# Kernel tuning notes

Hardware: AMD Instinct MI355X
Metric: run time of the kernel (lower is better)

## Reference

```python
import jax, jax.numpy as jnp
import numpy as np


def setup_inputs() -> dict:
    key = jax.random.key(0)
    ks = jax.random.split(key, 8)
    B, H, W, C = 4, 64, 64, 256
    d = C // 8  # 32
    s = 0.02
    return {
        "x": jax.random.normal(ks[0], (B, H, W, C), dtype=jnp.float32),
        "Wq": jax.random.normal(ks[1], (C, d), dtype=jnp.float32) * s,
        "bq": jnp.zeros((d,), dtype=jnp.float32),
        "Wk": jax.random.normal(ks[2], (C, d), dtype=jnp.float32) * s,
        "bk": jnp.zeros((d,), dtype=jnp.float32),
        "Wv": jax.random.normal(ks[3], (C, C), dtype=jnp.float32) * s,
        "bv": jnp.zeros((C,), dtype=jnp.float32),
        "gamma": jnp.zeros((1,), dtype=jnp.float32),
    }


def reference(x, Wq, bq, Wk, bk, Wv, bv, gamma):
    B, H, W, C = x.shape
    N = H * W
    xf = x.reshape(B, N, C)                       # 1x1 conv == per-pixel matmul
    q = xf @ Wq + bq                              # [B, N, C//8]
    k = xf @ Wk + bk                              # [B, N, C//8]
    v = xf @ Wv + bv                              # [B, N, C]
    attn = jax.nn.softmax(jnp.einsum('bnd,bmd->bnm', q, k), axis=-1)  # [B, N, N]
    out = jnp.einsum('bnm,bmc->bnc', attn, v).reshape(B, H, W, C)
    return gamma * out + x
```

## Files before the change

### kernel.cpp

```cpp
#include <hip/hip_runtime.h>
#include <hip/hip_bf16.h>

typedef __bf16 bf16;
typedef __bf16 bf16x8 __attribute__((ext_vector_type(8)));
typedef __bf16 bf16x4 __attribute__((ext_vector_type(4)));
typedef float f32x4 __attribute__((ext_vector_type(4)));

static __device__ __forceinline__ f32x4 mfma16(bf16x8 a, bf16x8 b, f32x4 c) {
  return __builtin_amdgcn_mfma_f32_16x16x32_bf16(a, b, c, 0, 0, 0);
}

static __device__ __forceinline__ void wg_barrier() {
  asm volatile("s_waitcnt lgkmcnt(0)" ::: "memory");
  __builtin_amdgcn_s_barrier();
  asm volatile("" ::: "memory");
}

static __device__ __forceinline__ bf16x8 cvt8(const float* p) {
  f32x4 a0 = *(const f32x4*)p;
  f32x4 a1 = *(const f32x4*)(p + 4);
  bf16x8 r;
#pragma unroll
  for (int j = 0; j < 4; ++j) { r[j] = (bf16)a0[j]; r[4 + j] = (bf16)a1[j]; }
  return r;
}

__global__ void prep_wt(const float* __restrict__ Wq, const float* __restrict__ Wk,
                        const float* __restrict__ Wv, bf16* __restrict__ Wf) {
  int k = blockIdx.x;
  int c = threadIdx.x;
  float v;
  if (c < 32)       v = Wq[k * 32 + c];
  else if (c < 64)  v = Wk[k * 32 + (c - 32)];
  else              v = Wv[k * 256 + (c - 64)];
  int t5 = c >> 6, ct = (c >> 4) & 3, lwc = c & 15;
  int kc = k >> 5, qq = (k >> 3) & 3, ke = k & 7;
  Wf[((((t5 * 8 + kc) * 4 + ct) * 64) + qq * 16 + lwc) * 8 + ke] = (bf16)v;
}

__global__ __launch_bounds__(256) void qkv_gemm(
    const float* __restrict__ x, const bf16* __restrict__ Wf,
    const float* __restrict__ bq, const float* __restrict__ bk,
    const float* __restrict__ bv,
    bf16* __restrict__ Qd, bf16* __restrict__ Kd, bf16* __restrict__ Vt) {
  __shared__ __align__(16) bf16 tile[64 * 72];
  int tid = threadIdx.x;
  int lane = tid & 63, w = tid >> 6;
  int lw = lane & 15, qq = lane >> 4;
  int r0 = blockIdx.x * 64;
  int bb = r0 >> 12, n0 = r0 & 4095;

  const float* arow = x + (size_t)(r0 + 16 * w + lw) * 256;
  bf16x8 a[8];
#pragma unroll
  for (int kc = 0; kc < 8; ++kc) a[kc] = cvt8(arow + kc * 32 + qq * 8);

  for (int c0 = 0; c0 < 320; c0 += 64) {
    int t5 = c0 >> 6;
    f32x4 acc[4] = {};
#pragma unroll
    for (int kc = 0; kc < 8; ++kc)
#pragma unroll
      for (int t = 0; t < 4; ++t) {
        bf16x8 b = *(const bf16x8*)(Wf + ((size_t)(((t5 * 8 + kc) * 4 + t) * 64) + lane) * 8);
        acc[t] = mfma16(a[kc], b, acc[t]);
      }
    if (c0 == 0) {
#pragma unroll
      for (int t = 0; t < 4; ++t) {
        int c = 16 * t + lw;
        float bias = (c < 32) ? bq[c] : bk[c - 32];
#pragma unroll
        for (int i = 0; i < 4; ++i) {
          int n = n0 + 16 * w + 4 * qq + i;
          bf16 hv = (bf16)(acc[t][i] + bias);
          if (c < 32) Qd[((size_t)(bb << 12) + n) * 32 + c] = hv;
          else        Kd[((size_t)(bb << 12) + n) * 32 + (c - 32)] = hv;
        }
      }
    } else {
#pragma unroll
      for (int t = 0; t < 4; ++t) {
        int cl = 16 * t + lw;
        float bias = bv[c0 - 64 + cl];
#pragma unroll
        for (int i = 0; i < 4; ++i)
          tile[cl * 72 + 16 * w + 4 * qq + i] = (bf16)(acc[t][i] + bias);
      }
      __syncthreads();
      int nl = tid & 63;
#pragma unroll
      for (int it = 0; it < 16; ++it) {
        int cl = 4 * it + w;
        Vt[((size_t)bb * 256 + (c0 - 64) + cl) * 4096 + n0 + nl] = tile[cl * 72 + nl];
      }
      __syncthreads();
    }
  }
}

__global__ __launch_bounds__(512, 2) void flash_attn(
    const bf16* __restrict__ Qd, const bf16* __restrict__ Kd,
    const bf16* __restrict__ Vt, const float* __restrict__ x,
    const float* __restrict__ gamma, float* __restrict__ out) {
  __shared__ __align__(16) bf16 Pl[2][64 * 136];
  __shared__ __align__(16) float lsum2[2][64];

  int tid = threadIdx.x;
  int lane = tid & 63, w = tid >> 6;
  int lw = lane & 15, qq = lane >> 4;
  int wr = w & 3, wc = w >> 2, chb = 32 * w;
  int bb = blockIdx.y;
  int r0 = blockIdx.x * 64;

  const bf16* Qb = Qd + ((size_t)bb << 12) * 32;
  const bf16* Kb = Kd + ((size_t)bb << 12) * 32;
  const bf16* Vb = Vt + (size_t)bb * 256 * 4096;

  bf16x8 qf = *(const bf16x8*)(Qb + (size_t)(r0 + 16 * wr + lw) * 32 + qq * 8);

  f32x4 o[4][2] = {};
  float l_acc = 0.f;
  bf16x8 kbuf0[4], kbuf1[4], vbuf0[8], vbuf1[8];

#pragma unroll
  for (int t = 0; t < 4; ++t)
    kbuf0[t] = *(const bf16x8*)(Kb + (size_t)(64 * wc + 16 * t + lw) * 32 + qq * 8);
#pragma unroll
  for (int t = 0; t < 4; ++t) {
    f32x4 z = {};
    f32x4 s = mfma16(kbuf0[t], qf, z);
    bf16x4 pk;
#pragma unroll
    for (int i = 0; i < 4; ++i) { float p = __expf(s[i]); l_acc += p; pk[i] = (bf16)p; }
    *(bf16x4*)&Pl[0][(16 * wr + lw) * 136 + 64 * wc + 16 * t + 4 * qq] = pk;
  }
#pragma unroll
  for (int t = 0; t < 4; ++t)
    kbuf1[t] = *(const bf16x8*)(Kb + (size_t)(128 + 64 * wc + 16 * t + lw) * 32 + qq * 8);
#pragma unroll
  for (int t = 0; t < 2; ++t)
#pragma unroll
    for (int kc = 0; kc < 4; ++kc)
      vbuf0[t * 4 + kc] = *(const bf16x8*)(Vb + (size_t)(chb + 16 * t + lw) * 4096 + kc * 32 + qq * 8);
  wg_barrier();

#define FA_BODY(J, PCUR, PNXT, KN, KC, VC, VN)                                     \
  {                                                                                \
    const int j = (J);                                                             \
    int n1 = ((j + 1) & 31) * 128, n2 = ((j + 2) & 31) * 128;                      \
    if (j < 31) {                                                                  \
      _Pragma("unroll") for (int t = 0; t < 4; ++t) {                              \
        f32x4 z = {};                                                              \
        f32x4 s = mfma16(KN[t], qf, z);                                            \
        bf16x4 pk;                                                                 \
        _Pragma("unroll") for (int i = 0; i < 4; ++i) {                            \
          float p = __expf(s[i]); l_acc += p; pk[i] = (bf16)p;                     \
        }                                                                          \
        *(bf16x4*)&Pl[PNXT][(16 * wr + lw) * 136 + 64 * wc + 16 * t + 4 * qq] = pk; \
      }                                                                            \
      _Pragma("unroll") for (int t = 0; t < 4; ++t)                                \
        KC[t] = *(const bf16x8*)(Kb + (size_t)(n2 + 64 * wc + 16 * t + lw) * 32 + qq * 8); \
    }                                                                              \
    _Pragma("unroll") for (int t = 0; t < 2; ++t)                                  \
      _Pragma("unroll") for (int kc = 0; kc < 4; ++kc)                             \
        VN[t * 4 + kc] = *(const bf16x8*)(Vb + (size_t)(chb + 16 * t + lw) * 4096 + n1 + kc * 32 + qq * 8); \
    _Pragma("unroll") for (int kc = 0; kc < 4; ++kc) {                             \
      bf16x8 afk[4];                                                               \
      _Pragma("unroll") for (int m = 0; m < 4; ++m)                                \
        afk[m] = *(const bf16x8*)&Pl[PCUR][(16 * m + lw) * 136 + kc * 32 + qq * 8]; \
      _Pragma("unroll") for (int t = 0; t < 2; ++t)                                \
        _Pragma("unroll") for (int m = 0; m < 4; ++m)                              \
          o[m][t] = mfma16(afk[m], VC[t * 4 + kc], o[m][t]);                       \
    }                                                                              \
    wg_barrier();                                                                  \
  }

  for (int jj = 0; jj < 16; ++jj) {
    FA_BODY(2 * jj,     0, 1, kbuf1, kbuf0, vbuf0, vbuf1)
    FA_BODY(2 * jj + 1, 1, 0, kbuf0, kbuf1, vbuf1, vbuf0)
  }
#undef FA_BODY

  l_acc += __shfl_xor(l_acc, 16);
  l_acc += __shfl_xor(l_acc, 32);
  if (qq == 0) lsum2[wc][16 * wr + lw] = l_acc;
  __syncthreads();

  float g = gamma[0];
#pragma unroll
  for (int m = 0; m < 4; ++m) {
    f32x4 la = *(const f32x4*)&lsum2[0][16 * m + 4 * qq];
    f32x4 lb = *(const f32x4*)&lsum2[1][16 * m + 4 * qq];
#pragma unroll
    for (int i = 0; i < 4; ++i) {
      float rinv = 1.f / (la[i] + lb[i]);
      int row = r0 + 16 * m + 4 * qq + i;
      size_t base = (((size_t)bb << 12) + row) * 256 + chb;
#pragma unroll
      for (int t = 0; t < 2; ++t)
        out[base + 16 * t + lw] = g * (o[m][t][i] * rinv) + x[base + 16 * t + lw];
    }
  }
}

extern "C" void kernel_launch(void* const* d_in, const int* in_sizes, int n_in,
                              void* d_out, int out_size, void* d_ws, size_t ws_size,
                              hipStream_t stream) {
  const float* x     = (const float*)d_in[0];
  const float* Wq    = (const float*)d_in[1];
  const float* bq    = (const float*)d_in[2];
  const float* Wk    = (const float*)d_in[3];
  const float* bk    = (const float*)d_in[4];
  const float* Wv    = (const float*)d_in[5];
  const float* bv    = (const float*)d_in[6];
  const float* gamma = (const float*)d_in[7];
  float* out = (float*)d_out;

  const size_t WT_E = 320 * 256;
  const size_t QK_E = (size_t)4096 * 32;
  const size_t VT_E = (size_t)256 * 4096;
  size_t full_bytes = (WT_E + 4 * 2 * QK_E + 4 * VT_E) * sizeof(bf16);

  bf16* Wf = (bf16*)d_ws;
  prep_wt<<<dim3(256), dim3(320), 0, stream>>>(Wq, Wk, Wv, Wf);

  if (ws_size >= full_bytes) {
    bf16* Qd = Wf + WT_E;
    bf16* Kd = Qd + 4 * QK_E;
    bf16* Vt = Kd + 4 * QK_E;
    qkv_gemm<<<dim3(256), dim3(256), 0, stream>>>(x, Wf, bq, bk, bv, Qd, Kd, Vt);
    flash_attn<<<dim3(64, 4), dim3(512), 0, stream>>>(Qd, Kd, Vt, x, gamma, out);
  } else {
    bf16* Qd = Wf + WT_E;
    bf16* Kd = Qd + QK_E;
    bf16* Vt = Kd + QK_E;
    for (int b = 0; b < 4; ++b) {
      const float* xb = x + (size_t)b * 4096 * 256;
      float* outb = out + (size_t)b * 4096 * 256;
      qkv_gemm<<<dim3(64), dim3(256), 0, stream>>>(xb, Wf, bq, bk, bv, Qd, Kd, Vt);
      flash_attn<<<dim3(64, 1), dim3(512), 0, stream>>>(Qd, Kd, Vt, xb, gamma, outb);
    }
  }
}
```

Measured before the change: 171.6 us.

## Split flash attention waves into producer (QK/exp) and consumer (PV) roles

Restructures the attention kernel so waves 0-3 compute QK^T scores and exp into a double-buffered LDS P tile, while waves 4-7 only run the PV MFMAs over 64-channel slices. The KV step shrinks from 128 to 64 keys, so there are twice as many barrier phases. The goal is to overlap the exp/VALU work with the matrix work across waves instead of serializing them inside each wave. The catch is that half the waves do only light work, so the kernel needs more barriers and carries a larger per-wave O accumulator, which raises register pressure.

```diff
diff --git a/kernel.cpp b/kernel.cpp
--- a/kernel.cpp
+++ b/kernel.cpp
@@ -103,13 +103,12 @@
     const bf16* __restrict__ Qd, const bf16* __restrict__ Kd,
     const bf16* __restrict__ Vt, const float* __restrict__ x,
     const float* __restrict__ gamma, float* __restrict__ out) {
-  __shared__ __align__(16) bf16 Pl[2][64 * 136];
-  __shared__ __align__(16) float lsum2[2][64];
+  __shared__ __align__(16) bf16 Pl[2][64 * 72];
+  __shared__ float lsum[4][64];
 
   int tid = threadIdx.x;
   int lane = tid & 63, w = tid >> 6;
   int lw = lane & 15, qq = lane >> 4;
-  int wr = w & 3, wc = w >> 2, chb = 32 * w;
   int bb = blockIdx.y;
   int r0 = blockIdx.x * 64;
 
@@ -117,89 +116,114 @@
   const bf16* Kb = Kd + ((size_t)bb << 12) * 32;
   const bf16* Vb = Vt + (size_t)bb * 256 * 4096;
 
-  bf16x8 qf = *(const bf16x8*)(Qb + (size_t)(r0 + 16 * wr + lw) * 32 + qq * 8);
-
-  f32x4 o[4][2] = {};
-  float l_acc = 0.f;
-  bf16x8 kbuf0[4], kbuf1[4], vbuf0[8], vbuf1[8];
-
-#pragma unroll
-  for (int t = 0; t < 4; ++t)
-    kbuf0[t] = *(const bf16x8*)(Kb + (size_t)(64 * wc + 16 * t + lw) * 32 + qq * 8);
-#pragma unroll
-  for (int t = 0; t < 4; ++t) {
-    f32x4 z = {};
-    f32x4 s = mfma16(kbuf0[t], qf, z);
-    bf16x4 pk;
-#pragma unroll
-    for (int i = 0; i < 4; ++i) { float p = __expf(s[i]); l_acc += p; pk[i] = (bf16)p; }
-    *(bf16x4*)&Pl[0][(16 * wr + lw) * 136 + 64 * wc + 16 * t + 4 * qq] = pk;
-  }
-#pragma unroll
-  for (int t = 0; t < 4; ++t)
-    kbuf1[t] = *(const bf16x8*)(Kb + (size_t)(128 + 64 * wc + 16 * t + lw) * 32 + qq * 8);
-#pragma unroll
-  for (int t = 0; t < 2; ++t)
-#pragma unroll
-    for (int kc = 0; kc < 4; ++kc)
-      vbuf0[t * 4 + kc] = *(const bf16x8*)(Vb + (size_t)(chb + 16 * t + lw) * 4096 + kc * 32 + qq * 8);
-  wg_barrier();
-
-#define FA_BODY(J, PCUR, PNXT, KN, KC, VC, VN)                                     \
-  {                                                                                \
-    const int j = (J);                                                             \
-    int n1 = ((j + 1) & 31) * 128, n2 = ((j + 2) & 31) * 128;                      \
-    if (j < 31) {                                                                  \
-      _Pragma("unroll") for (int t = 0; t < 4; ++t) {                              \
-        f32x4 z = {};                                                              \
-        f32x4 s = mfma16(KN[t], qf, z);                                            \
-        bf16x4 pk;                                                                 \
-        _Pragma("unroll") for (int i = 0; i < 4; ++i) {                            \
-          float p = __expf(s[i]); l_acc += p; pk[i] = (bf16)p;                     \
-        }                                                                          \
-        *(bf16x4*)&Pl[PNXT][(16 * wr + lw) * 136 + 64 * wc + 16 * t + 4 * qq] = pk; \
-      }                                                                            \
-      _Pragma("unroll") for (int t = 0; t < 4; ++t)                                \
-        KC[t] = *(const bf16x8*)(Kb + (size_t)(n2 + 64 * wc + 16 * t + lw) * 32 + qq * 8); \
-    }                                                                              \
-    _Pragma("unroll") for (int t = 0; t < 2; ++t)                                  \
-      _Pragma("unroll") for (int kc = 0; kc < 4; ++kc)                             \
-        VN[t * 4 + kc] = *(const bf16x8*)(Vb + (size_t)(chb + 16 * t + lw) * 4096 + n1 + kc * 32 + qq * 8); \
-    _Pragma("unroll") for (int kc = 0; kc < 4; ++kc) {                             \
-      bf16x8 afk[4];                                                               \
-      _Pragma("unroll") for (int m = 0; m < 4; ++m)                                \
-        afk[m] = *(const bf16x8*)&Pl[PCUR][(16 * m + lw) * 136 + kc * 32 + qq * 8]; \
-      _Pragma("unroll") for (int t = 0; t < 2; ++t)                                \
-        _Pragma("unroll") for (int m = 0; m < 4; ++m)                              \
-          o[m][t] = mfma16(afk[m], VC[t * 4 + kc], o[m][t]);                       \
-    }                                                                              \
-    wg_barrier();                                                                  \
-  }
-
-  for (int jj = 0; jj < 16; ++jj) {
-    FA_BODY(2 * jj,     0, 1, kbuf1, kbuf0, vbuf0, vbuf1)
-    FA_BODY(2 * jj + 1, 1, 0, kbuf0, kbuf1, vbuf1, vbuf0)
-  }
-#undef FA_BODY
-
-  l_acc += __shfl_xor(l_acc, 16);
-  l_acc += __shfl_xor(l_acc, 32);
-  if (qq == 0) lsum2[wc][16 * wr + lw] = l_acc;
-  __syncthreads();
-
-  float g = gamma[0];
-#pragma unroll
-  for (int m = 0; m < 4; ++m) {
-    f32x4 la = *(const f32x4*)&lsum2[0][16 * m + 4 * qq];
-    f32x4 lb = *(const f32x4*)&lsum2[1][16 * m + 4 * qq];
-#pragma unroll
-    for (int i = 0; i < 4; ++i) {
-      float rinv = 1.f / (la[i] + lb[i]);
-      int row = r0 + 16 * m + 4 * qq + i;
-      size_t base = (((size_t)bb << 12) + row) * 256 + chb;
-#pragma unroll
-      for (int t = 0; t < 2; ++t)
-        out[base + 16 * t + lw] = g * (o[m][t][i] * rinv) + x[base + 16 * t + lw];
+  if (w < 4) {
+    int kvs = 16 * w;
+    bf16x8 qfp[4];
+#pragma unroll
+    for (int qt = 0; qt < 4; ++qt)
+      qfp[qt] = *(const bf16x8*)(Qb + (size_t)(r0 + 16 * qt + lw) * 32 + qq * 8);
+    float l_part[4] = {};
+    bf16x8 kA, kB;
+
+    kA = *(const bf16x8*)(Kb + (size_t)(kvs + lw) * 32 + qq * 8);
+#pragma unroll
+    for (int qt = 0; qt < 4; ++qt) {
+      f32x4 z = {};
+      f32x4 s = mfma16(kA, qfp[qt], z);
+      bf16x4 pk;
+#pragma unroll
+      for (int i = 0; i < 4; ++i) { float p = __expf(s[i]); l_part[qt] += p; pk[i] = (bf16)p; }
+      *(bf16x4*)&Pl[0][(16 * qt + lw) * 72 + kvs + 4 * qq] = pk;
+    }
+    kB = *(const bf16x8*)(Kb + (size_t)(64 + kvs + lw) * 32 + qq * 8);
+    wg_barrier();
+
+#define PROD_PH(J, PN, KC, KN)                                                 \
+    {                                                                          \
+      const int j = (J);                                                       \
+      if (j < 63) {                                                            \
+        _Pragma("unroll") for (int qt = 0; qt < 4; ++qt) {                     \
+          f32x4 z = {};                                                        \
+          f32x4 s = mfma16(KC, qfp[qt], z);                                    \
+          bf16x4 pk;                                                           \
+          _Pragma("unroll") for (int i = 0; i < 4; ++i) {                      \
+            float p = __expf(s[i]); l_part[qt] += p; pk[i] = (bf16)p;          \
+          }                                                                    \
+          *(bf16x4*)&Pl[PN][(16 * qt + lw) * 72 + kvs + 4 * qq] = pk;          \
+        }                                                                      \
+        int n2 = ((j + 2) & 63) * 64;                                          \
+        KN = *(const bf16x8*)(Kb + (size_t)(n2 + kvs + lw) * 32 + qq * 8);     \
+      }                                                                        \
+      wg_barrier();                                                            \
+    }
+
+    for (int jj = 0; jj < 32; ++jj) {
+      PROD_PH(2 * jj,     1, kB, kA)
+      PROD_PH(2 * jj + 1, 0, kA, kB)
+    }
+#undef PROD_PH
+
+#pragma unroll
+    for (int qt = 0; qt < 4; ++qt) {
+      float v = l_part[qt];
+      v += __shfl_xor(v, 16);
+      v += __shfl_xor(v, 32);
+      if (qq == 0) lsum[w][16 * qt + lw] = v;
+    }
+    __syncthreads();
+  } else {
+    int chb = 64 * (w - 4);
+    f32x4 o[4][4] = {};
+    bf16x8 vA[8], vB[8];
+#pragma unroll
+    for (int t = 0; t < 4; ++t)
+#pragma unroll
+      for (int kc = 0; kc < 2; ++kc)
+        vA[t * 2 + kc] = *(const bf16x8*)(Vb + (size_t)(chb + 16 * t + lw) * 4096 + kc * 32 + qq * 8);
+    wg_barrier();
+
+#define CONS_PH(J, PC, VC, VN)                                                 \
+    {                                                                          \
+      const int j = (J);                                                       \
+      int n1 = ((j + 1) & 63) * 64;                                            \
+      bf16x8 af[4][2];                                                         \
+      _Pragma("unroll") for (int m = 0; m < 4; ++m)                            \
+        _Pragma("unroll") for (int kc = 0; kc < 2; ++kc)                       \
+          af[m][kc] = *(const bf16x8*)&Pl[PC][(16 * m + lw) * 72 + kc * 32 + qq * 8]; \
+      _Pragma("unroll") for (int t = 0; t < 4; ++t)                            \
+        _Pragma("unroll") for (int kc = 0; kc < 2; ++kc)                       \
+          VN[t * 2 + kc] = *(const bf16x8*)(Vb + (size_t)(chb + 16 * t + lw) * 4096 + n1 + kc * 32 + qq * 8); \
+      _Pragma("unroll") for (int kc = 0; kc < 2; ++kc)                         \
+        _Pragma("unroll") for (int t = 0; t < 4; ++t)                          \
+          _Pragma("unroll") for (int m = 0; m < 4; ++m)                        \
+            o[m][t] = mfma16(af[m][kc], VC[t * 2 + kc], o[m][t]);              \
+      wg_barrier();                                                            \
+    }
+
+    for (int jj = 0; jj < 32; ++jj) {
+      CONS_PH(2 * jj,     0, vA, vB)
+      CONS_PH(2 * jj + 1, 1, vB, vA)
+    }
+#undef CONS_PH
+
+    __syncthreads();
+
+    float g = gamma[0];
+#pragma unroll
+    for (int m = 0; m < 4; ++m) {
+      f32x4 l0 = *(const f32x4*)&lsum[0][16 * m + 4 * qq];
+      f32x4 l1 = *(const f32x4*)&lsum[1][16 * m + 4 * qq];
+      f32x4 l2 = *(const f32x4*)&lsum[2][16 * m + 4 * qq];
+      f32x4 l3 = *(const f32x4*)&lsum[3][16 * m + 4 * qq];
+#pragma unroll
+      for (int i = 0; i < 4; ++i) {
+        float rinv = 1.f / (l0[i] + l1[i] + l2[i] + l3[i]);
+        int row = r0 + 16 * m + 4 * qq + i;
+        size_t base = (((size_t)bb << 12) + row) * 256 + chb;
+#pragma unroll
+        for (int t = 0; t < 4; ++t)
+          out[base + 16 * t + lw] = g * (o[m][t][i] * rinv) + x[base + 16 * t + lw];
+      }
     }
   }
 }
```

Measured after the change: 159.3 us. 7.2% less time.
